# Performance work log

Hardware: AMD Instinct MI355X
Metric: run time of the kernel (lower is better)

The kernel has to match this reference:

```python
import jax, jax.numpy as jnp
import numpy as np

N = 40000          # nodes
E = 640000         # edges (avg degree 16)
F_IN = 128         # num_node_features
H = 64             # hidden_channels
C_OUT = 32         # num_classes


def _glorot(key, fan_in, fan_out):
    lim = np.sqrt(6.0 / (fan_in + fan_out)).astype(np.float32)
    return jax.random.uniform(key, (fan_in, fan_out), jnp.float32, -lim, lim)


def setup_inputs() -> dict:
    key = jax.random.key(0)
    ks = jax.random.split(key, 12)
    x = jax.random.normal(ks[0], (N, F_IN), jnp.float32)
    edge_index = jax.random.randint(ks[1], (2, E), 0, N, dtype=jnp.int32)
    batch = jnp.zeros((N,), jnp.int32)  # unused by forward, kept for signature fidelity
    return {
        "x": x,
        "edge_index": edge_index,
        "batch": batch,
        "W1": _glorot(ks[2], F_IN, H),      "b1": jnp.zeros((H,), jnp.float32),
        "W2": _glorot(ks[3], H, 2 * H),     "b2": jnp.zeros((2 * H,), jnp.float32),
        "W3": _glorot(ks[4], 2 * H, 2 * H), "b3": jnp.zeros((2 * H,), jnp.float32),
        "W4": _glorot(ks[5], 2 * H, H),     "b4": jnp.zeros((H,), jnp.float32),
        "Wl": _glorot(ks[6], H, C_OUT),     "bl": jnp.zeros((C_OUT,), jnp.float32),
    }


def _gcn_norm(edge_index, n_nodes):
    """Add self-loops and compute symmetric D^{-1/2} A D^{-1/2} edge weights."""
    loop = jnp.arange(n_nodes, dtype=edge_index.dtype)
    src = jnp.concatenate([edge_index[0], loop])
    dst = jnp.concatenate([edge_index[1], loop])
    deg = jax.ops.segment_sum(jnp.ones_like(dst, dtype=jnp.float32), dst,
                              num_segments=n_nodes)
    d_inv_sqrt = jnp.where(deg > 0, jax.lax.rsqrt(deg), 0.0)
    norm = d_inv_sqrt[src] * d_inv_sqrt[dst]  # [E + N]
    return src, dst, norm


def _gcn_conv(h, W, b, src, dst, norm, n_nodes):
    h = h @ W                                   # [N, d_out] linear transform first
    msg = h[src] * norm[:, None]                # gather + edge scaling
    agg = jax.ops.segment_sum(msg, dst, num_segments=n_nodes)  # scatter-add
    return agg + b


def reference(x, edge_index, batch, W1, b1, W2, b2, W3, b3, W4, b4, Wl, bl):
    n_nodes = x.shape[0]
    src, dst, norm = _gcn_norm(edge_index, n_nodes)
    # eval mode: F.dropout(training=False) is identity
    h = jax.nn.relu(_gcn_conv(x, W1, b1, src, dst, norm, n_nodes))
    h = jax.nn.relu(_gcn_conv(h, W2, b2, src, dst, norm, n_nodes))
    h = jax.nn.relu(_gcn_conv(h, W3, b3, src, dst, norm, n_nodes))
    h = jax.nn.relu(_gcn_conv(h, W4, b4, src, dst, norm, n_nodes))
    return h @ Wl + bl  # [N, C_OUT]
```

## Files before the change

kernel.cpp:

```cpp
#include <hip/hip_runtime.h>
#include <hip/hip_bf16.h>


using bf16x8 = __attribute__((ext_vector_type(8))) __bf16;
using f32x4  = __attribute__((ext_vector_type(4))) float;

__device__ __forceinline__ int block_detect_bf16(const unsigned short* __restrict__ x16) {
    __shared__ int cnt;
    if (threadIdx.x == 0) cnt = 0;
    __syncthreads();
    if (threadIdx.x < 128) {
        unsigned e = (x16[2 * threadIdx.x] >> 7) & 0xFF;
        if (e >= 100 && e <= 135) atomicAdd(&cnt, 1);
    }
    __syncthreads();
    return cnt >= 64;
}

struct PrepDesc { const void* src; void* dst; int n; int mode; int dol2; int strideK; };
struct PrepArgs { PrepDesc d[12]; int pre[13]; int ndesc; };

__global__ __launch_bounds__(256) void setup(PrepArgs a,
                                             const unsigned short* __restrict__ x16,
                                             int* __restrict__ flagG,
                                             const int* __restrict__ dstE,
                                             int* __restrict__ count, int E) {
    const int b = blockIdx.x;
    const int npre = a.pre[a.ndesc];
    if (b >= npre) {
        int e = (b - npre) * 256 + threadIdx.x;
        if (e < E) atomicAdd(&count[dstE[e]], 1);
        return;
    }
    const int fl = block_detect_bf16(x16);
    if (b == 0 && threadIdx.x == 0) *flagG = fl;
    int s = 0;
    for (; s < a.ndesc - 1; ++s) if (b < a.pre[s + 1]) break;
    const PrepDesc d = a.d[s];
    int i = (b - a.pre[s]) * 256 + threadIdx.x;
    if (i >= d.n) return;
    float v = fl ? __bfloat162float(((const __hip_bfloat16*)d.src)[i])
                 : ((const float*)d.src)[i];
    if (d.mode == 0) {
        ((float*)d.dst)[i] = v;
    } else {
        int k = i >> d.dol2;
        int col = i & ((1 << d.dol2) - 1);
        ((__hip_bfloat16*)d.dst)[col * d.strideK + k] = __float2bfloat16(v);
    }
}

__global__ __launch_bounds__(256) void scan_part(const int* __restrict__ count,
                                                 int* __restrict__ blockSums, int N) {
    __shared__ int red[256];
    const int t = threadIdx.x;
    const int i = (blockIdx.x << 8) + t;
    red[t] = (i < N) ? (count[i] + 7) & ~7 : 0;
    __syncthreads();
    for (int off = 128; off > 0; off >>= 1) {
        if (t < off) red[t] += red[t + off];
        __syncthreads();
    }
    if (t == 0) blockSums[blockIdx.x] = red[0];
}

__global__ __launch_bounds__(256) void scan_final(const int* __restrict__ count,
                                                  const int* __restrict__ blockSums,
                                                  int* __restrict__ rowptr,
                                                  int* __restrict__ bukCursor,
                                                  float* __restrict__ dinv,
                                                  int N) {
    __shared__ int lds[256];
    __shared__ int sOff;
    const int t = threadIdx.x;
    const int i = (blockIdx.x << 8) + t;
    const int c = (i < N) ? count[i] : 0;
    const int cp = (c + 7) & ~7;
    lds[t] = cp;
    __syncthreads();
    for (int off = 1; off < 256; off <<= 1) {
        int v = (t >= off) ? lds[t - off] : 0;
        __syncthreads();
        lds[t] += v;
        __syncthreads();
    }
    if (t == 0) {
        int o = 0;
        for (int b = 0; b < (int)blockIdx.x; ++b) o += blockSums[b];
        sOff = o;
    }
    __syncthreads();
    const int run = sOff + lds[t] - cp;
    if (i < N) {
        rowptr[i] = run;
        dinv[i] = rsqrtf((float)(c + 1));
        if ((i & 255) == 0) bukCursor[i >> 8] = run;
        if (i == N - 1) rowptr[N] = run + cp;
    }
}

__global__ __launch_bounds__(256) void bucket_scatter(const unsigned* __restrict__ staging,
                                                      const int* __restrict__ bukCursor,
                                                      const int* __restrict__ rowptr,
                                                      unsigned short* __restrict__ csr16,
                                                      int N) {
    __shared__ int cur[256];
    const int t = threadIdx.x;
    const int nb0 = blockIdx.x << 8;
    const int i = nb0 + t;
    cur[t] = (i < N) ? rowptr[i] : 0;
    __syncthreads();
    const int base = rowptr[nb0];
    const int m = bukCursor[blockIdx.x] - base;
    for (int k = t; k < m; k += 256) {
        unsigned e = staging[base + k];
        int loc = (e >> 16) & 255;
        int pos = atomicAdd(&cur[loc], 1);
        csr16[pos] = (unsigned short)(e & 0xffff);
    }
    __syncthreads();
    if (i < N) {
        const int end = rowptr[i + 1];
        for (int p = cur[t]; p < end; ++p) csr16[p] = (unsigned short)N;
    }
}

template<int W>
__device__ __forceinline__ void gather_acc8(const __hip_bfloat16* __restrict__ Hin,
                                            int cb, int node,
                                            const int* __restrict__ rowptr,
                                            const unsigned short* __restrict__ csr16,
                                            float acc[8]) {
    const __hip_bfloat16* base = Hin + cb;
    auto loadrow = [&](int s) -> uint4 {
        return *(const uint4*)(base + (size_t)s * W);
    };
    #pragma unroll
    for (int j = 0; j < 8; ++j) acc[j] = 0.f;
    auto accum = [&](uint4 u) {
        union { uint4 v; __hip_bfloat162 h2[4]; } c;
        c.v = u;
        #pragma unroll
        for (int j = 0; j < 4; ++j) {
            float2 p = __bfloat1622float2(c.h2[j]);
            acc[2 * j] += p.x;
            acc[2 * j + 1] += p.y;
        }
    };
    accum(loadrow(node));
    int e = rowptr[node];
    const int e1 = rowptr[node + 1];
    for (; e + 16 <= e1; e += 16) {
        union { uint4 v; unsigned short s[8]; } iv0, iv1;
        iv0.v = *(const uint4*)(csr16 + e);
        iv1.v = *(const uint4*)(csr16 + e + 8);
        uint4 r0 = loadrow(iv0.s[0]), r1 = loadrow(iv0.s[1]);
        uint4 r2 = loadrow(iv0.s[2]), r3 = loadrow(iv0.s[3]);
        uint4 r4 = loadrow(iv0.s[4]), r5 = loadrow(iv0.s[5]);
        uint4 r6 = loadrow(iv0.s[6]), r7 = loadrow(iv0.s[7]);
        uint4 r8 = loadrow(iv1.s[0]), r9 = loadrow(iv1.s[1]);
        uint4 ra = loadrow(iv1.s[2]), rb = loadrow(iv1.s[3]);
        uint4 rc = loadrow(iv1.s[4]), rd = loadrow(iv1.s[5]);
        uint4 re = loadrow(iv1.s[6]), rf = loadrow(iv1.s[7]);
        accum(r0); accum(r1); accum(r2); accum(r3);
        accum(r4); accum(r5); accum(r6); accum(r7);
        accum(r8); accum(r9); accum(ra); accum(rb);
        accum(rc); accum(rd); accum(re); accum(rf);
    }
    if (e < e1) {
        union { uint4 v; unsigned short s[8]; } iv;
        iv.v = *(const uint4*)(csr16 + e);
        uint4 r0 = loadrow(iv.s[0]), r1 = loadrow(iv.s[1]);
        uint4 r2 = loadrow(iv.s[2]), r3 = loadrow(iv.s[3]);
        uint4 r4 = loadrow(iv.s[4]), r5 = loadrow(iv.s[5]);
        uint4 r6 = loadrow(iv.s[6]), r7 = loadrow(iv.s[7]);
        accum(r0); accum(r1); accum(r2); accum(r3);
        accum(r4); accum(r5); accum(r6); accum(r7);
    }
}

__device__ __forceinline__ void zero_pad_row_b(__hip_bfloat16* zrow, int zn, bool lead) {
    if (zrow && lead) {
        for (int i = threadIdx.x * 8; i < zn; i += 2048)
            *(uint4*)(zrow + i) = make_uint4(0, 0, 0, 0);
    }
}

template<bool BIAS_RELU, bool POST_SCALE>
__global__ __launch_bounds__(256) void gather8(const __hip_bfloat16* __restrict__ Hin,
                                               const int* __restrict__ rowptr,
                                               const unsigned short* __restrict__ csr16,
                                               const float* __restrict__ dinv,
                                               const float* __restrict__ b,
                                               __hip_bfloat16* __restrict__ out, int n,
                                               __hip_bfloat16* zrow, int zn) {
    zero_pad_row_b(zrow, zn, blockIdx.x == 0);
    const int t = blockIdx.x * 256 + threadIdx.x;
    const int node = t >> 3;
    const int f = t & 7;
    if (node >= n) return;
    const int cb = f * 8;
    const float di = dinv[node];
    float acc[8];
    gather_acc8<64>(Hin, cb, node, rowptr, csr16, acc);
    union { uint4 v; __hip_bfloat16 h[8]; } p;
    #pragma unroll
    for (int j = 0; j < 8; ++j) {
        float v = di * acc[j];
        if (BIAS_RELU) v = fmaxf(v + b[cb + j], 0.f);
        if (POST_SCALE) v *= di;
        p.h[j] = __float2bfloat16(v);
    }
    *(uint4*)(out + (size_t)node * 64 + cb) = p.v;
}

template<int NTPW, bool BIAS_RELU, bool SCALE_ROW, bool RAW_A>
__device__ __forceinline__ void gemm_core(const void* __restrict__ Ain,
                                          const __hip_bfloat16* __restrict__ WT,
                                          const float* __restrict__ bias,
                                          const float* __restrict__ dinv,
                                          __hip_bfloat16* __restrict__ out,
                                          int d_in, int d_out_log2, int strideK,
                                          bool bfmode, int blk, int tid) {
    const int wave = tid >> 6, lane = tid & 63;
    const int m = lane & 15, quad = lane >> 4;
    const int rowBase = blk * 64;
    const int nkc = d_in >> 5;
    const int nt0 = wave * NTPW;

    f32x4 acc[4][NTPW];
    #pragma unroll
    for (int rt = 0; rt < 4; ++rt)
        #pragma unroll
        for (int j = 0; j < NTPW; ++j)
            acc[rt][j] = (f32x4){0.f, 0.f, 0.f, 0.f};

    auto mainloop = [&](bool asBF) {
        for (int kc = 0; kc < nkc; ++kc) {
            const int koff = (kc << 5) + quad * 8;
            bf16x8 a[4];
            #pragma unroll
            for (int rt = 0; rt < 4; ++rt) {
                const size_t off = (size_t)(rowBase + rt * 16 + m) * d_in + koff;
                if (!RAW_A || asBF) {
                    a[rt] = *(const bf16x8*)((const __hip_bfloat16*)Ain + off);
                } else {
                    const float* p = (const float*)Ain + off;
                    float4 f0 = *(const float4*)p;
                    float4 f1 = *(const float4*)(p + 4);
                    union { bf16x8 v; __hip_bfloat16 h[8]; } u;
                    u.h[0] = __float2bfloat16(f0.x); u.h[1] = __float2bfloat16(f0.y);
                    u.h[2] = __float2bfloat16(f0.z); u.h[3] = __float2bfloat16(f0.w);
                    u.h[4] = __float2bfloat16(f1.x); u.h[5] = __float2bfloat16(f1.y);
                    u.h[6] = __float2bfloat16(f1.z); u.h[7] = __float2bfloat16(f1.w);
                    a[rt] = u.v;
                }
            }
            #pragma unroll
            for (int j = 0; j < NTPW; ++j) {
                const int n = ((nt0 + j) << 4) + m;
                bf16x8 b = *(const bf16x8*)&WT[n * strideK + koff];
                #pragma unroll
                for (int rt = 0; rt < 4; ++rt)
                    acc[rt][j] = __builtin_amdgcn_mfma_f32_16x16x32_bf16(a[rt], b, acc[rt][j], 0, 0, 0);
            }
        }
    };
    if (bfmode) mainloop(true); else mainloop(false);

    const int d_out = 1 << d_out_log2;
    #pragma unroll
    for (int rt = 0; rt < 4; ++rt) {
        const int row = rowBase + rt * 16 + quad * 4;
        #pragma unroll
        for (int j = 0; j < NTPW; ++j) {
            const int col = ((nt0 + j) << 4) + m;
            float bv = BIAS_RELU ? bias[col] : 0.f;
            #pragma unroll
            for (int r = 0; r < 4; ++r) {
                float v = acc[rt][j][r];
                if (BIAS_RELU) v = fmaxf(v + bv, 0.f);
                if (SCALE_ROW) v *= dinv[row + r];
                out[(size_t)(row + r) * d_out + col] = __float2bfloat16(v);
            }
        }
    }
}

__global__ __launch_bounds__(256) void stage_gemm(const int* __restrict__ src,
                                                  const int* __restrict__ dst,
                                                  int E, int NBUK,
                                                  int* __restrict__ bukCursor,
                                                  unsigned* __restrict__ staging,
                                                  const void* __restrict__ Ain,
                                                  const __hip_bfloat16* __restrict__ WT,
                                                  const float* __restrict__ dinv,
                                                  __hip_bfloat16* __restrict__ out,
                                                  int strideK, const int* __restrict__ flag,
                                                  __hip_bfloat16* zrow, int zn, int SB) {
    if (blockIdx.x < SB) {
        __shared__ int hist[160], start[160], run[160];
        const int t = threadIdx.x;
        const int base = blockIdx.x * 4096;
        int sv[16], dv[16];
        #pragma unroll
        for (int j = 0; j < 16; ++j) {
            int e = base + j * 256 + t;
            if (e < E) { sv[j] = src[e]; dv[j] = dst[e]; } else dv[j] = -1;
        }
        if (t < NBUK) { hist[t] = 0; run[t] = 0; }
        __syncthreads();
        #pragma unroll
        for (int j = 0; j < 16; ++j)
            if (dv[j] >= 0) atomicAdd(&hist[dv[j] >> 8], 1);
        __syncthreads();
        if (t < NBUK && hist[t] > 0)
            start[t] = atomicAdd(&bukCursor[t], hist[t]);
        __syncthreads();
        #pragma unroll
        for (int j = 0; j < 16; ++j) {
            if (dv[j] >= 0) {
                int b = dv[j] >> 8;
                int slot = start[b] + atomicAdd(&run[b], 1);
                staging[slot] = ((unsigned)dv[j] << 16) | (unsigned)sv[j];
            }
        }
        return;
    }
    const int blk = blockIdx.x - SB;
    zero_pad_row_b(zrow, zn, blk == 0);
    const bool bfmode = (*flag != 0);
    gemm_core<1, false, true, true>(Ain, WT, nullptr, dinv, out, 128, 6, strideK,
                                    bfmode, blk, threadIdx.x);
}

template<int D_IN, int NTPW, bool BIAS_RELU, bool SCALE_ROW>
__global__ __launch_bounds__(256) void gather_gemm(const __hip_bfloat16* __restrict__ Hin,
                                                   const int* __restrict__ rowptr,
                                                   const unsigned short* __restrict__ csr16,
                                                   const float* __restrict__ dinv,
                                                   const __hip_bfloat16* __restrict__ WT,
                                                   const float* __restrict__ bias,
                                                   __hip_bfloat16* __restrict__ out,
                                                   int d_out_log2,
                                                   __hip_bfloat16* zrow, int zn) {
    zero_pad_row_b(zrow, zn, blockIdx.x == 0);
    constexpr int SK = D_IN + 8;
    __shared__ __align__(16) __hip_bfloat16 sG[64 * SK];
    const int tid = threadIdx.x;

    const int rowBase = blockIdx.x * 64;
    constexpr int TPR = D_IN / 8;
    constexpr int NPP = 256 / TPR;
    #pragma unroll
    for (int pass = 0; pass < 64 / NPP; ++pass) {
        const int local = pass * NPP + tid / TPR;
        const int node = rowBase + local;
        const int cb = (tid % TPR) * 8;
        float acc[8];
        gather_acc8<D_IN>(Hin, cb, node, rowptr, csr16, acc);
        const float di = dinv[node];
        union { bf16x8 v; __hip_bfloat16 h[8]; } p;
        #pragma unroll
        for (int j = 0; j < 8; ++j) p.h[j] = __float2bfloat16(di * acc[j]);
        *(bf16x8*)&sG[local * SK + cb] = p.v;
    }
    __syncthreads();

    const int wave = tid >> 6, lane = tid & 63;
    const int m = lane & 15, quad = lane >> 4;
    const int nkc = D_IN >> 5;
    const int nt0 = wave * NTPW;

    f32x4 acc2[4][NTPW];
    #pragma unroll
    for (int rt = 0; rt < 4; ++rt)
        #pragma unroll
        for (int j = 0; j < NTPW; ++j)
            acc2[rt][j] = (f32x4){0.f, 0.f, 0.f, 0.f};

    for (int kc = 0; kc < nkc; ++kc) {
        const int koff = (kc << 5) + quad * 8;
        bf16x8 a[4];
        #pragma unroll
        for (int rt = 0; rt < 4; ++rt)
            a[rt] = *(const bf16x8*)&sG[(rt * 16 + m) * SK + koff];
        #pragma unroll
        for (int j = 0; j < NTPW; ++j) {
            const int n = ((nt0 + j) << 4) + m;
            bf16x8 b = *(const bf16x8*)&WT[n * SK + koff];
            #pragma unroll
            for (int rt = 0; rt < 4; ++rt)
                acc2[rt][j] = __builtin_amdgcn_mfma_f32_16x16x32_bf16(a[rt], b, acc2[rt][j], 0, 0, 0);
        }
    }

    const int d_out = 1 << d_out_log2;
    #pragma unroll
    for (int rt = 0; rt < 4; ++rt) {
        const int row = rowBase + rt * 16 + quad * 4;
        #pragma unroll
        for (int j = 0; j < NTPW; ++j) {
            const int col = ((nt0 + j) << 4) + m;
            float bv = BIAS_RELU ? bias[col] : 0.f;
            #pragma unroll
            for (int r = 0; r < 4; ++r) {
                float v = acc2[rt][j][r];
                if (BIAS_RELU) v = fmaxf(v + bv, 0.f);
                if (SCALE_ROW) v *= dinv[row + r];
                out[(size_t)(row + r) * d_out + col] = __float2bfloat16(v);
            }
        }
    }
}

__global__ __launch_bounds__(256) void gather_gemm34(const __hip_bfloat16* __restrict__ Hin,
                                                     const int* __restrict__ rowptr,
                                                     const unsigned short* __restrict__ csr16,
                                                     const float* __restrict__ dinv,
                                                     const __hip_bfloat16* __restrict__ WT3,
                                                     const float* __restrict__ b3,
                                                     const __hip_bfloat16* __restrict__ WT4,
                                                     __hip_bfloat16* __restrict__ lin4,
                                                     __hip_bfloat16* zrow, int zn) {
    zero_pad_row_b(zrow, zn, blockIdx.x == 0);
    constexpr int SK = 136;
    __shared__ __align__(16) __hip_bfloat16 sG[64 * SK];
    const int tid = threadIdx.x;
    const int rowBase = blockIdx.x * 64;

    #pragma unroll
    for (int pass = 0; pass < 4; ++pass) {
        const int local = pass * 16 + tid / 16;
        const int node = rowBase + local;
        const int cb = (tid % 16) * 8;
        float acc[8];
        gather_acc8<128>(Hin, cb, node, rowptr, csr16, acc);
        const float di = dinv[node];
        union { bf16x8 v; __hip_bfloat16 h[8]; } p;
        #pragma unroll
        for (int j = 0; j < 8; ++j) p.h[j] = __float2bfloat16(di * acc[j]);
        *(bf16x8*)&sG[local * SK + cb] = p.v;
    }
    __syncthreads();

    const int wave = tid >> 6, lane = tid & 63;
    const int m = lane & 15, quad = lane >> 4;

    f32x4 acc2[4][2];
    #pragma unroll
    for (int rt = 0; rt < 4; ++rt)
        #pragma unroll
        for (int j = 0; j < 2; ++j)
            acc2[rt][j] = (f32x4){0.f, 0.f, 0.f, 0.f};
    for (int kc = 0; kc < 4; ++kc) {
        const int koff = (kc << 5) + quad * 8;
        bf16x8 a[4];
        #pragma unroll
        for (int rt = 0; rt < 4; ++rt)
            a[rt] = *(const bf16x8*)&sG[(rt * 16 + m) * SK + koff];
        #pragma unroll
        for (int j = 0; j < 2; ++j) {
            const int n = ((wave * 2 + j) << 4) + m;
            bf16x8 b = *(const bf16x8*)&WT3[n * SK + koff];
            #pragma unroll
            for (int rt = 0; rt < 4; ++rt)
                acc2[rt][j] = __builtin_amdgcn_mfma_f32_16x16x32_bf16(a[rt], b, acc2[rt][j], 0, 0, 0);
        }
    }
    __syncthreads();

    #pragma unroll
    for (int j = 0; j < 2; ++j) {
        const int col = ((wave * 2 + j) << 4) + m;
        const float bv = b3[col];
        #pragma unroll
        for (int rt = 0; rt < 4; ++rt) {
            const int row = rt * 16 + quad * 4;
            #pragma unroll
            for (int r = 0; r < 4; ++r)
                sG[(row + r) * SK + col] = __float2bfloat16(fmaxf(acc2[rt][j][r] + bv, 0.f));
        }
    }
    __syncthreads();

    f32x4 acc3[4];
    #pragma unroll
    for (int rt = 0; rt < 4; ++rt) acc3[rt] = (f32x4){0.f, 0.f, 0.f, 0.f};
    for (int kc = 0; kc < 4; ++kc) {
        const int koff = (kc << 5) + quad * 8;
        bf16x8 a[4];
        #pragma unroll
        for (int rt = 0; rt < 4; ++rt)
            a[rt] = *(const bf16x8*)&sG[(rt * 16 + m) * SK + koff];
        const int n = (wave << 4) + m;
        bf16x8 b = *(const bf16x8*)&WT4[n * SK + koff];
        #pragma unroll
        for (int rt = 0; rt < 4; ++rt)
            acc3[rt] = __builtin_amdgcn_mfma_f32_16x16x32_bf16(a[rt], b, acc3[rt], 0, 0, 0);
    }

    const int col = (wave << 4) + m;
    #pragma unroll
    for (int rt = 0; rt < 4; ++rt) {
        const int row = rowBase + rt * 16 + quad * 4;
        #pragma unroll
        for (int r = 0; r < 4; ++r)
            lin4[(size_t)(row + r) * 64 + col] = __float2bfloat16(acc3[rt][r] * dinv[row + r]);
    }
}

__global__ __launch_bounds__(256) void gather_final(const __hip_bfloat16* __restrict__ Hin,
                                                    const int* __restrict__ rowptr,
                                                    const unsigned short* __restrict__ csr16,
                                                    const float* __restrict__ dinv,
                                                    const float* __restrict__ b4,
                                                    const float* __restrict__ Wlf,
                                                    const float* __restrict__ blf,
                                                    void* __restrict__ out,
                                                    const int* __restrict__ flag) {
    __shared__ float sWl[64 * 32];
    __shared__ float sH[32 * 65];
    const int tid = threadIdx.x;
    for (int i = tid; i < 2048; i += 256) sWl[i] = Wlf[i];
    const int nl = tid >> 3, j = tid & 7, cb = j * 8;
    const int node = blockIdx.x * 32 + nl;
    float acc[8];
    gather_acc8<64>(Hin, cb, node, rowptr, csr16, acc);
    const float di = dinv[node];
    #pragma unroll
    for (int k = 0; k < 8; ++k)
        sH[nl * 65 + cb + k] = fmaxf(di * acc[k] + b4[cb + k], 0.f);
    __syncthreads();
    float4 r = *(const float4*)(blf + 4 * j);
    for (int k = 0; k < 64; ++k) {
        const float hv = sH[nl * 65 + k];
        const float4 w = *(const float4*)&sWl[k * 32 + 4 * j];
        r.x += hv * w.x; r.y += hv * w.y; r.z += hv * w.z; r.w += hv * w.w;
    }
    const size_t idx = (size_t)node * 32 + 4 * j;
    if (*flag) {
        union { __hip_bfloat16 h[4]; uint2 u; } p;
        p.h[0] = __float2bfloat16(r.x); p.h[1] = __float2bfloat16(r.y);
        p.h[2] = __float2bfloat16(r.z); p.h[3] = __float2bfloat16(r.w);
        *(uint2*)((__hip_bfloat16*)out + idx) = p.u;
    } else {
        *(float4*)((float*)out + idx) = r;
    }
}

extern "C" void kernel_launch(void* const* d_in, const int* in_sizes, int n_in,
                              void* d_out, int out_size, void* d_ws, size_t ws_size,
                              hipStream_t stream) {
    const int* edge = (const int*)d_in[1];
    const int F_IN = 128;
    const int N = in_sizes[0] / F_IN;
    const int E = in_sizes[1] / 2;
    const int* src = edge;
    const int* dst = edge + E;
    const int NBUK = (N + 255) >> 8;

    auto align256 = [](size_t v) { return (v + 255) & ~(size_t)255; };
    char* ws = (char*)d_ws;
    int*   flag    = (int*)ws;    ws += 256;
    float* dinv    = (float*)ws;  ws += align256((size_t)N * 4);
    int*   count   = (int*)ws;    ws += align256((size_t)N * 4);
    int*   rowptr  = (int*)ws;    ws += align256((size_t)(N + 1) * 4);
    int*   bukCursor = (int*)ws;  ws += align256((size_t)NBUK * 4);
    int*   blockSums = (int*)ws;  ws += align256((size_t)NBUK * 4);
    unsigned short* csr16 = (unsigned short*)ws; ws += align256(((size_t)E + 8 * N + 64) * 2);
    unsigned* staging = (unsigned*)ws; ws += align256(((size_t)E + 8 * N + 64) * 4);
    __hip_bfloat16* Hbuf = (__hip_bfloat16*)ws; ws += align256(((size_t)N + 1) * 128 * 2);
    __hip_bfloat16* Tbuf = (__hip_bfloat16*)ws; ws += align256(((size_t)N + 1) * 128 * 2);

    const int widx[4] = {3, 5, 7, 9};
    const int bidx[4] = {4, 6, 8, 10};
    float* Bc[4];
    for (int i = 0; i < 4; ++i) { Bc[i] = (float*)ws; ws += align256((size_t)in_sizes[bidx[i]] * 4); }
    float* Wlf = (float*)ws; ws += align256((size_t)in_sizes[11] * 4);
    float* blf = (float*)ws; ws += align256((size_t)in_sizes[12] * 4);

    const int LD_IN[4]  = {128, 64, 128, 128};
    const int LD_OL2[4] = {6, 7, 7, 6};
    int strideK[4];
    __hip_bfloat16* WT[4];
    for (int l = 0; l < 4; ++l) {
        strideK[l] = LD_IN[l] + 8;
        WT[l] = (__hip_bfloat16*)ws;
        ws += align256((size_t)(1 << LD_OL2[l]) * strideK[l] * 2);
    }

    hipMemsetAsync(count, 0, (size_t)N * 4, stream);

    PrepArgs pa{};
    int nd = 0, pre = 0;
    auto addDesc = [&](const void* s, void* d, int n, int mode, int dol2, int sk) {
        pa.d[nd] = {s, d, n, mode, dol2, sk};
        pa.pre[nd] = pre;
        pre += (n + 255) / 256;
        nd++;
    };
    for (int l = 0; l < 4; ++l)
        addDesc(d_in[widx[l]], WT[l], LD_IN[l] << LD_OL2[l], 1, LD_OL2[l], strideK[l]);
    for (int l = 0; l < 4; ++l)
        addDesc(d_in[bidx[l]], Bc[l], in_sizes[bidx[l]], 0, 0, 0);
    addDesc(d_in[11], Wlf, in_sizes[11], 0, 0, 0);
    addDesc(d_in[12], blf, in_sizes[12], 0, 0, 0);
    pa.pre[nd] = pre;
    pa.ndesc = nd;
    const int EB = (E + 255) / 256;
    setup<<<pre + EB, 256, 0, stream>>>(pa, (const unsigned short*)d_in[0], flag, dst, count, E);

    scan_part<<<NBUK, 256, 0, stream>>>(count, blockSums, N);
    scan_final<<<NBUK, 256, 0, stream>>>(count, blockSums, rowptr, bukCursor, dinv, N);

    const int nblk = N / 64;
    const int g64  = (N * 8 + 255) / 256;
    const int SB   = (E + 4095) / 4096;

    stage_gemm<<<SB + nblk, 256, 0, stream>>>(
        src, dst, E, NBUK, bukCursor, staging,
        d_in[0], WT[0], dinv, Tbuf, strideK[0], flag, Tbuf + (size_t)N * 64, 64, SB);

    bucket_scatter<<<NBUK, 256, 0, stream>>>(staging, bukCursor, rowptr, csr16, N);

    gather8<true, true><<<g64, 256, 0, stream>>>(
        Tbuf, rowptr, csr16, dinv, Bc[0], Hbuf, N, Hbuf + (size_t)N * 64, 64);

    gather_gemm<64, 2, true, true><<<nblk, 256, 0, stream>>>(
        Hbuf, rowptr, csr16, dinv, WT[1], Bc[1], Tbuf, 7, Tbuf + (size_t)N * 128, 128);

    gather_gemm34<<<nblk, 256, 0, stream>>>(
        Tbuf, rowptr, csr16, dinv, WT[2], Bc[2], WT[3], Hbuf,
        Hbuf + (size_t)N * 64, 64);

    gather_final<<<g64, 256, 0, stream>>>(
        Hbuf, rowptr, csr16, dinv, Bc[3], Wlf, blf, d_out, flag);
}
```

Baseline: 220.8 us.

## Bucket edges by fixed-capacity buckets, fuse CSR build, store per-edge norm weights

The CSR build is reorganised. Edges are binned into fixed-capacity per-bucket staging regions first. The degree histogram, dinv and block sums are then computed from those buckets in the same launch as the first GEMM, and the scan and scatter are merged into one kernel. This removes the global count atomics and several launches. The CSR entries grow from 16 to 32 bits and carry a bf16 copy of the source node's dinv, so the gathers apply per-edge weights instead of relying on pre-scaled rows. That doubles index traffic, rounds the weights to bf16, and assumes each bucket fits within BUKCAP.

Result: faster. 200.9 us (-9.0%).

```diff
diff --git a/kernel.cpp b/kernel.cpp
--- a/kernel.cpp
+++ b/kernel.cpp
@@ -4,6 +4,8 @@
 
 using bf16x8 = __attribute__((ext_vector_type(8))) __bf16;
 using f32x4  = __attribute__((ext_vector_type(4))) float;
+
+#define BUKCAP 8192
 
 __device__ __forceinline__ int block_detect_bf16(const unsigned short* __restrict__ x16) {
     __shared__ int cnt;
@@ -20,16 +22,43 @@
 struct PrepDesc { const void* src; void* dst; int n; int mode; int dol2; int strideK; };
 struct PrepArgs { PrepDesc d[12]; int pre[13]; int ndesc; };
 
-__global__ __launch_bounds__(256) void setup(PrepArgs a,
-                                             const unsigned short* __restrict__ x16,
-                                             int* __restrict__ flagG,
-                                             const int* __restrict__ dstE,
-                                             int* __restrict__ count, int E) {
+__global__ __launch_bounds__(256) void prep_stage(PrepArgs a,
+                                                  const unsigned short* __restrict__ x16,
+                                                  int* __restrict__ flagG,
+                                                  const int* __restrict__ src,
+                                                  const int* __restrict__ dst,
+                                                  int E, int NBUK,
+                                                  int* __restrict__ bukFill,
+                                                  unsigned* __restrict__ staging) {
     const int b = blockIdx.x;
     const int npre = a.pre[a.ndesc];
     if (b >= npre) {
-        int e = (b - npre) * 256 + threadIdx.x;
-        if (e < E) atomicAdd(&count[dstE[e]], 1);
+        __shared__ int hist[160], start[160], run[160];
+        const int t = threadIdx.x;
+        const int base = (b - npre) * 4096;
+        int sv[16], dv[16];
+        #pragma unroll
+        for (int j = 0; j < 16; ++j) {
+            int e = base + j * 256 + t;
+            if (e < E) { sv[j] = src[e]; dv[j] = dst[e]; } else dv[j] = -1;
+        }
+        if (t < NBUK) { hist[t] = 0; run[t] = 0; }
+        __syncthreads();
+        #pragma unroll
+        for (int j = 0; j < 16; ++j)
+            if (dv[j] >= 0) atomicAdd(&hist[dv[j] >> 8], 1);
+        __syncthreads();
+        if (t < NBUK && hist[t] > 0)
+            start[t] = atomicAdd(&bukFill[t], hist[t]);
+        __syncthreads();
+        #pragma unroll
+        for (int j = 0; j < 16; ++j) {
+            if (dv[j] >= 0) {
+                int bk = dv[j] >> 8;
+                int slot = start[bk] + atomicAdd(&run[bk], 1);
+                staging[(size_t)bk * BUKCAP + slot] = ((unsigned)dv[j] << 16) | (unsigned)sv[j];
+            }
+        }
         return;
     }
     const int fl = block_detect_bf16(x16);
@@ -50,175 +79,10 @@
     }
 }
 
-__global__ __launch_bounds__(256) void scan_part(const int* __restrict__ count,
-                                                 int* __restrict__ blockSums, int N) {
-    __shared__ int red[256];
-    const int t = threadIdx.x;
-    const int i = (blockIdx.x << 8) + t;
-    red[t] = (i < N) ? (count[i] + 7) & ~7 : 0;
-    __syncthreads();
-    for (int off = 128; off > 0; off >>= 1) {
-        if (t < off) red[t] += red[t + off];
-        __syncthreads();
-    }
-    if (t == 0) blockSums[blockIdx.x] = red[0];
-}
-
-__global__ __launch_bounds__(256) void scan_final(const int* __restrict__ count,
-                                                  const int* __restrict__ blockSums,
-                                                  int* __restrict__ rowptr,
-                                                  int* __restrict__ bukCursor,
-                                                  float* __restrict__ dinv,
-                                                  int N) {
-    __shared__ int lds[256];
-    __shared__ int sOff;
-    const int t = threadIdx.x;
-    const int i = (blockIdx.x << 8) + t;
-    const int c = (i < N) ? count[i] : 0;
-    const int cp = (c + 7) & ~7;
-    lds[t] = cp;
-    __syncthreads();
-    for (int off = 1; off < 256; off <<= 1) {
-        int v = (t >= off) ? lds[t - off] : 0;
-        __syncthreads();
-        lds[t] += v;
-        __syncthreads();
-    }
-    if (t == 0) {
-        int o = 0;
-        for (int b = 0; b < (int)blockIdx.x; ++b) o += blockSums[b];
-        sOff = o;
-    }
-    __syncthreads();
-    const int run = sOff + lds[t] - cp;
-    if (i < N) {
-        rowptr[i] = run;
-        dinv[i] = rsqrtf((float)(c + 1));
-        if ((i & 255) == 0) bukCursor[i >> 8] = run;
-        if (i == N - 1) rowptr[N] = run + cp;
-    }
-}
-
-__global__ __launch_bounds__(256) void bucket_scatter(const unsigned* __restrict__ staging,
-                                                      const int* __restrict__ bukCursor,
-                                                      const int* __restrict__ rowptr,
-                                                      unsigned short* __restrict__ csr16,
-                                                      int N) {
-    __shared__ int cur[256];
-    const int t = threadIdx.x;
-    const int nb0 = blockIdx.x << 8;
-    const int i = nb0 + t;
-    cur[t] = (i < N) ? rowptr[i] : 0;
-    __syncthreads();
-    const int base = rowptr[nb0];
-    const int m = bukCursor[blockIdx.x] - base;
-    for (int k = t; k < m; k += 256) {
-        unsigned e = staging[base + k];
-        int loc = (e >> 16) & 255;
-        int pos = atomicAdd(&cur[loc], 1);
-        csr16[pos] = (unsigned short)(e & 0xffff);
-    }
-    __syncthreads();
-    if (i < N) {
-        const int end = rowptr[i + 1];
-        for (int p = cur[t]; p < end; ++p) csr16[p] = (unsigned short)N;
-    }
-}
-
-template<int W>
-__device__ __forceinline__ void gather_acc8(const __hip_bfloat16* __restrict__ Hin,
-                                            int cb, int node,
-                                            const int* __restrict__ rowptr,
-                                            const unsigned short* __restrict__ csr16,
-                                            float acc[8]) {
-    const __hip_bfloat16* base = Hin + cb;
-    auto loadrow = [&](int s) -> uint4 {
-        return *(const uint4*)(base + (size_t)s * W);
-    };
-    #pragma unroll
-    for (int j = 0; j < 8; ++j) acc[j] = 0.f;
-    auto accum = [&](uint4 u) {
-        union { uint4 v; __hip_bfloat162 h2[4]; } c;
-        c.v = u;
-        #pragma unroll
-        for (int j = 0; j < 4; ++j) {
-            float2 p = __bfloat1622float2(c.h2[j]);
-            acc[2 * j] += p.x;
-            acc[2 * j + 1] += p.y;
-        }
-    };
-    accum(loadrow(node));
-    int e = rowptr[node];
-    const int e1 = rowptr[node + 1];
-    for (; e + 16 <= e1; e += 16) {
-        union { uint4 v; unsigned short s[8]; } iv0, iv1;
-        iv0.v = *(const uint4*)(csr16 + e);
-        iv1.v = *(const uint4*)(csr16 + e + 8);
-        uint4 r0 = loadrow(iv0.s[0]), r1 = loadrow(iv0.s[1]);
-        uint4 r2 = loadrow(iv0.s[2]), r3 = loadrow(iv0.s[3]);
-        uint4 r4 = loadrow(iv0.s[4]), r5 = loadrow(iv0.s[5]);
-        uint4 r6 = loadrow(iv0.s[6]), r7 = loadrow(iv0.s[7]);
-        uint4 r8 = loadrow(iv1.s[0]), r9 = loadrow(iv1.s[1]);
-        uint4 ra = loadrow(iv1.s[2]), rb = loadrow(iv1.s[3]);
-        uint4 rc = loadrow(iv1.s[4]), rd = loadrow(iv1.s[5]);
-        uint4 re = loadrow(iv1.s[6]), rf = loadrow(iv1.s[7]);
-        accum(r0); accum(r1); accum(r2); accum(r3);
-        accum(r4); accum(r5); accum(r6); accum(r7);
-        accum(r8); accum(r9); accum(ra); accum(rb);
-        accum(rc); accum(rd); accum(re); accum(rf);
-    }
-    if (e < e1) {
-        union { uint4 v; unsigned short s[8]; } iv;
-        iv.v = *(const uint4*)(csr16 + e);
-        uint4 r0 = loadrow(iv.s[0]), r1 = loadrow(iv.s[1]);
-        uint4 r2 = loadrow(iv.s[2]), r3 = loadrow(iv.s[3]);
-        uint4 r4 = loadrow(iv.s[4]), r5 = loadrow(iv.s[5]);
-        uint4 r6 = loadrow(iv.s[6]), r7 = loadrow(iv.s[7]);
-        accum(r0); accum(r1); accum(r2); accum(r3);
-        accum(r4); accum(r5); accum(r6); accum(r7);
-    }
-}
-
-__device__ __forceinline__ void zero_pad_row_b(__hip_bfloat16* zrow, int zn, bool lead) {
-    if (zrow && lead) {
-        for (int i = threadIdx.x * 8; i < zn; i += 2048)
-            *(uint4*)(zrow + i) = make_uint4(0, 0, 0, 0);
-    }
-}
-
-template<bool BIAS_RELU, bool POST_SCALE>
-__global__ __launch_bounds__(256) void gather8(const __hip_bfloat16* __restrict__ Hin,
-                                               const int* __restrict__ rowptr,
-                                               const unsigned short* __restrict__ csr16,
-                                               const float* __restrict__ dinv,
-                                               const float* __restrict__ b,
-                                               __hip_bfloat16* __restrict__ out, int n,
-                                               __hip_bfloat16* zrow, int zn) {
-    zero_pad_row_b(zrow, zn, blockIdx.x == 0);
-    const int t = blockIdx.x * 256 + threadIdx.x;
-    const int node = t >> 3;
-    const int f = t & 7;
-    if (node >= n) return;
-    const int cb = f * 8;
-    const float di = dinv[node];
-    float acc[8];
-    gather_acc8<64>(Hin, cb, node, rowptr, csr16, acc);
-    union { uint4 v; __hip_bfloat16 h[8]; } p;
-    #pragma unroll
-    for (int j = 0; j < 8; ++j) {
-        float v = di * acc[j];
-        if (BIAS_RELU) v = fmaxf(v + b[cb + j], 0.f);
-        if (POST_SCALE) v *= di;
-        p.h[j] = __float2bfloat16(v);
-    }
-    *(uint4*)(out + (size_t)node * 64 + cb) = p.v;
-}
-
-template<int NTPW, bool BIAS_RELU, bool SCALE_ROW, bool RAW_A>
+template<int NTPW, bool BIAS_RELU, bool RAW_A>
 __device__ __forceinline__ void gemm_core(const void* __restrict__ Ain,
                                           const __hip_bfloat16* __restrict__ WT,
                                           const float* __restrict__ bias,
-                                          const float* __restrict__ dinv,
                                           __hip_bfloat16* __restrict__ out,
                                           int d_in, int d_out_log2, int strideK,
                                           bool bfmode, int blk, int tid) {
@@ -280,75 +144,190 @@
             for (int r = 0; r < 4; ++r) {
                 float v = acc[rt][j][r];
                 if (BIAS_RELU) v = fmaxf(v + bv, 0.f);
-                if (SCALE_ROW) v *= dinv[row + r];
                 out[(size_t)(row + r) * d_out + col] = __float2bfloat16(v);
             }
         }
     }
 }
 
-__global__ __launch_bounds__(256) void stage_gemm(const int* __restrict__ src,
-                                                  const int* __restrict__ dst,
-                                                  int E, int NBUK,
-                                                  int* __restrict__ bukCursor,
-                                                  unsigned* __restrict__ staging,
-                                                  const void* __restrict__ Ain,
-                                                  const __hip_bfloat16* __restrict__ WT,
-                                                  const float* __restrict__ dinv,
-                                                  __hip_bfloat16* __restrict__ out,
-                                                  int strideK, const int* __restrict__ flag,
-                                                  __hip_bfloat16* zrow, int zn, int SB) {
-    if (blockIdx.x < SB) {
-        __shared__ int hist[160], start[160], run[160];
+__global__ __launch_bounds__(256) void hist_gemm(const unsigned* __restrict__ staging,
+                                                 const int* __restrict__ bukFill,
+                                                 int* __restrict__ count,
+                                                 float* __restrict__ dinv,
+                                                 int* __restrict__ blockSums,
+                                                 int N, int NBUK,
+                                                 const void* __restrict__ x,
+                                                 const __hip_bfloat16* __restrict__ WT0,
+                                                 __hip_bfloat16* __restrict__ lin1,
+                                                 int strideK0,
+                                                 const int* __restrict__ flag) {
+    if ((int)blockIdx.x < NBUK) {
+        __shared__ int hist[256];
+        __shared__ int red[256];
         const int t = threadIdx.x;
-        const int base = blockIdx.x * 4096;
-        int sv[16], dv[16];
-        #pragma unroll
-        for (int j = 0; j < 16; ++j) {
-            int e = base + j * 256 + t;
-            if (e < E) { sv[j] = src[e]; dv[j] = dst[e]; } else dv[j] = -1;
-        }
-        if (t < NBUK) { hist[t] = 0; run[t] = 0; }
-        __syncthreads();
-        #pragma unroll
-        for (int j = 0; j < 16; ++j)
-            if (dv[j] >= 0) atomicAdd(&hist[dv[j] >> 8], 1);
-        __syncthreads();
-        if (t < NBUK && hist[t] > 0)
-            start[t] = atomicAdd(&bukCursor[t], hist[t]);
-        __syncthreads();
-        #pragma unroll
-        for (int j = 0; j < 16; ++j) {
-            if (dv[j] >= 0) {
-                int b = dv[j] >> 8;
-                int slot = start[b] + atomicAdd(&run[b], 1);
-                staging[slot] = ((unsigned)dv[j] << 16) | (unsigned)sv[j];
-            }
-        }
+        hist[t] = 0;
+        __syncthreads();
+        const int fill = bukFill[blockIdx.x];
+        const unsigned* st = staging + (size_t)blockIdx.x * BUKCAP;
+        for (int k = t; k < fill; k += 256)
+            atomicAdd(&hist[(st[k] >> 16) & 255], 1);
+        __syncthreads();
+        const int i = (blockIdx.x << 8) + t;
+        const int c = hist[t];
+        if (i < N) {
+            count[i] = c;
+            dinv[i] = rsqrtf((float)(c + 1));
+        }
+        red[t] = (i < N) ? (c + 7) & ~7 : 0;
+        __syncthreads();
+        for (int off = 128; off > 0; off >>= 1) {
+            if (t < off) red[t] += red[t + off];
+            __syncthreads();
+        }
+        if (t == 0) blockSums[blockIdx.x] = red[0];
         return;
     }
-    const int blk = blockIdx.x - SB;
-    zero_pad_row_b(zrow, zn, blk == 0);
-    const bool bfmode = (*flag != 0);
-    gemm_core<1, false, true, true>(Ain, WT, nullptr, dinv, out, 128, 6, strideK,
-                                    bfmode, blk, threadIdx.x);
-}
-
-template<int D_IN, int NTPW, bool BIAS_RELU, bool SCALE_ROW>
+    gemm_core<1, false, true>(x, WT0, nullptr, lin1, 128, 6, strideK0,
+                              (*flag != 0), blockIdx.x - NBUK, threadIdx.x);
+}
+
+__global__ __launch_bounds__(256) void scan_scatter(const int* __restrict__ count,
+                                                    const int* __restrict__ blockSums,
+                                                    const int* __restrict__ bukFill,
+                                                    const unsigned* __restrict__ staging,
+                                                    const float* __restrict__ dinv,
+                                                    int* __restrict__ rowptr,
+                                                    unsigned* __restrict__ csr32,
+                                                    int N) {
+    __shared__ int lds[256];
+    __shared__ int cur[256];
+    __shared__ int sOff;
+    const int t = threadIdx.x;
+    const int i = (blockIdx.x << 8) + t;
+    const int c = (i < N) ? count[i] : 0;
+    const int cp = (c + 7) & ~7;
+    lds[t] = cp;
+    __syncthreads();
+    for (int off = 1; off < 256; off <<= 1) {
+        int v = (t >= off) ? lds[t - off] : 0;
+        __syncthreads();
+        lds[t] += v;
+        __syncthreads();
+    }
+    if (t == 0) {
+        int o = 0;
+        for (int b = 0; b < (int)blockIdx.x; ++b) o += blockSums[b];
+        sOff = o;
+    }
+    __syncthreads();
+    const int run = sOff + lds[t] - cp;
+    cur[t] = run;
+    if (i < N) {
+        rowptr[i] = run;
+        if (i == N - 1) rowptr[N] = run + cp;
+    }
+    __syncthreads();
+    const int fill = bukFill[blockIdx.x];
+    const unsigned* st = staging + (size_t)blockIdx.x * BUKCAP;
+    for (int k = t; k < fill; k += 256) {
+        unsigned u = st[k];
+        int s = (int)(u & 0xffffu);
+        int loc = (u >> 16) & 255;
+        int pos = atomicAdd(&cur[loc], 1);
+        union { __hip_bfloat16 h; unsigned short w16; } cv;
+        cv.h = __float2bfloat16(dinv[s]);
+        csr32[pos] = ((unsigned)cv.w16 << 16) | (unsigned)s;
+    }
+    __syncthreads();
+    const int pe = run + cp;
+    for (int p = cur[t]; p < pe; ++p) csr32[p] = 0u;
+}
+
+template<int W>
+__device__ __forceinline__ void gather_acc8w(const __hip_bfloat16* __restrict__ Hin,
+                                             int cb, int node, float di,
+                                             const int* __restrict__ rowptr,
+                                             const unsigned* __restrict__ csr32,
+                                             float acc[8]) {
+    const __hip_bfloat16* base = Hin + cb;
+    auto loadrow = [&](unsigned u) -> uint4 {
+        return *(const uint4*)(base + (size_t)(u & 0xffffu) * W);
+    };
+    auto wof = [](unsigned u) -> float {
+        return __int_as_float((int)(u & 0xffff0000u));
+    };
+    auto accumw = [&](uint4 v, float w) {
+        union { uint4 q; __hip_bfloat162 h2[4]; } c;
+        c.q = v;
+        #pragma unroll
+        for (int j = 0; j < 4; ++j) {
+            float2 p = __bfloat1622float2(c.h2[j]);
+            acc[2 * j]     += w * p.x;
+            acc[2 * j + 1] += w * p.y;
+        }
+    };
+    #pragma unroll
+    for (int j = 0; j < 8; ++j) acc[j] = 0.f;
+    accumw(*(const uint4*)(base + (size_t)node * W), di);
+    int e = rowptr[node];
+    const int e1 = rowptr[node + 1];
+    for (; e + 16 <= e1; e += 16) {
+        uint4 i0 = *(const uint4*)(csr32 + e);
+        uint4 i1 = *(const uint4*)(csr32 + e + 4);
+        uint4 i2 = *(const uint4*)(csr32 + e + 8);
+        uint4 i3 = *(const uint4*)(csr32 + e + 12);
+        uint4 r0 = loadrow(i0.x), r1 = loadrow(i0.y), r2 = loadrow(i0.z), r3 = loadrow(i0.w);
+        uint4 r4 = loadrow(i1.x), r5 = loadrow(i1.y), r6 = loadrow(i1.z), r7 = loadrow(i1.w);
+        uint4 r8 = loadrow(i2.x), r9 = loadrow(i2.y), ra = loadrow(i2.z), rb = loadrow(i2.w);
+        uint4 rc = loadrow(i3.x), rd = loadrow(i3.y), re = loadrow(i3.z), rf = loadrow(i3.w);
+        accumw(r0, wof(i0.x)); accumw(r1, wof(i0.y)); accumw(r2, wof(i0.z)); accumw(r3, wof(i0.w));
+        accumw(r4, wof(i1.x)); accumw(r5, wof(i1.y)); accumw(r6, wof(i1.z)); accumw(r7, wof(i1.w));
+        accumw(r8, wof(i2.x)); accumw(r9, wof(i2.y)); accumw(ra, wof(i2.z)); accumw(rb, wof(i2.w));
+        accumw(rc, wof(i3.x)); accumw(rd, wof(i3.y)); accumw(re, wof(i3.z)); accumw(rf, wof(i3.w));
+    }
+    if (e < e1) {
+        uint4 i0 = *(const uint4*)(csr32 + e);
+        uint4 i1 = *(const uint4*)(csr32 + e + 4);
+        uint4 r0 = loadrow(i0.x), r1 = loadrow(i0.y), r2 = loadrow(i0.z), r3 = loadrow(i0.w);
+        uint4 r4 = loadrow(i1.x), r5 = loadrow(i1.y), r6 = loadrow(i1.z), r7 = loadrow(i1.w);
+        accumw(r0, wof(i0.x)); accumw(r1, wof(i0.y)); accumw(r2, wof(i0.z)); accumw(r3, wof(i0.w));
+        accumw(r4, wof(i1.x)); accumw(r5, wof(i1.y)); accumw(r6, wof(i1.z)); accumw(r7, wof(i1.w));
+    }
+}
+
+__global__ __launch_bounds__(256) void gather8(const __hip_bfloat16* __restrict__ Hin,
+                                               const int* __restrict__ rowptr,
+                                               const unsigned* __restrict__ csr32,
+                                               const float* __restrict__ dinv,
+                                               const float* __restrict__ b,
+                                               __hip_bfloat16* __restrict__ out, int n) {
+    const int t = blockIdx.x * 256 + threadIdx.x;
+    const int node = t >> 3;
+    const int f = t & 7;
+    if (node >= n) return;
+    const int cb = f * 8;
+    const float di = dinv[node];
+    float acc[8];
+    gather_acc8w<64>(Hin, cb, node, di, rowptr, csr32, acc);
+    union { uint4 v; __hip_bfloat16 h[8]; } p;
+    #pragma unroll
+    for (int j = 0; j < 8; ++j)
+        p.h[j] = __float2bfloat16(fmaxf(di * acc[j] + b[cb + j], 0.f));
+    *(uint4*)(out + (size_t)node * 64 + cb) = p.v;
+}
+
+template<int D_IN, int NTPW>
 __global__ __launch_bounds__(256) void gather_gemm(const __hip_bfloat16* __restrict__ Hin,
                                                    const int* __restrict__ rowptr,
-                                                   const unsigned short* __restrict__ csr16,
+                                                   const unsigned* __restrict__ csr32,
                                                    const float* __restrict__ dinv,
                                                    const __hip_bfloat16* __restrict__ WT,
                                                    const float* __restrict__ bias,
                                                    __hip_bfloat16* __restrict__ out,
-                                                   int d_out_log2,
-                                                   __hip_bfloat16* zrow, int zn) {
-    zero_pad_row_b(zrow, zn, blockIdx.x == 0);
+                                                   int d_out_log2) {
     constexpr int SK = D_IN + 8;
     __shared__ __align__(16) __hip_bfloat16 sG[64 * SK];
     const int tid = threadIdx.x;
-
     const int rowBase = blockIdx.x * 64;
     constexpr int TPR = D_IN / 8;
     constexpr int NPP = 256 / TPR;
@@ -357,9 +336,9 @@
         const int local = pass * NPP + tid / TPR;
         const int node = rowBase + local;
         const int cb = (tid % TPR) * 8;
+        const float di = dinv[node];
         float acc[8];
-        gather_acc8<D_IN>(Hin, cb, node, rowptr, csr16, acc);
-        const float di = dinv[node];
+        gather_acc8w<D_IN>(Hin, cb, node, di, rowptr, csr32, acc);
         union { bf16x8 v; __hip_bfloat16 h[8]; } p;
         #pragma unroll
         for (int j = 0; j < 8; ++j) p.h[j] = __float2bfloat16(di * acc[j]);
@@ -402,28 +381,23 @@
         #pragma unroll
         for (int j = 0; j < NTPW; ++j) {
             const int col = ((nt0 + j) << 4) + m;
-            float bv = BIAS_RELU ? bias[col] : 0.f;
+            const float bv = bias[col];
             #pragma unroll
-            for (int r = 0; r < 4; ++r) {
-                float v = acc2[rt][j][r];
-                if (BIAS_RELU) v = fmaxf(v + bv, 0.f);
-                if (SCALE_ROW) v *= dinv[row + r];
-                out[(size_t)(row + r) * d_out + col] = __float2bfloat16(v);
-            }
+            for (int r = 0; r < 4; ++r)
+                out[(size_t)(row + r) * d_out + col] =
+                    __float2bfloat16(fmaxf(acc2[rt][j][r] + bv, 0.f));
         }
     }
 }
 
 __global__ __launch_bounds__(256) void gather_gemm34(const __hip_bfloat16* __restrict__ Hin,
                                                      const int* __restrict__ rowptr,
-                                                     const unsigned short* __restrict__ csr16,
+                                                     const unsigned* __restrict__ csr32,
                                                      const float* __restrict__ dinv,
                                                      const __hip_bfloat16* __restrict__ WT3,
                                                      const float* __restrict__ b3,
                                                      const __hip_bfloat16* __restrict__ WT4,
-                                                     __hip_bfloat16* __restrict__ lin4,
-                                                     __hip_bfloat16* zrow, int zn) {
-    zero_pad_row_b(zrow, zn, blockIdx.x == 0);
+                                                     __hip_bfloat16* __restrict__ lin4) {
     constexpr int SK = 136;
     __shared__ __align__(16) __hip_bfloat16 sG[64 * SK];
     const int tid = threadIdx.x;
@@ -434,9 +408,9 @@
         const int local = pass * 16 + tid / 16;
         const int node = rowBase + local;
         const int cb = (tid % 16) * 8;
+        const float di = dinv[node];
         float acc[8];
-        gather_acc8<128>(Hin, cb, node, rowptr, csr16, acc);
-        const float di = dinv[node];
+        gather_acc8w<128>(Hin, cb, node, di, rowptr, csr32, acc);
         union { bf16x8 v; __hip_bfloat16 h[8]; } p;
         #pragma unroll
         for (int j = 0; j < 8; ++j) p.h[j] = __float2bfloat16(di * acc[j]);
@@ -499,20 +473,19 @@
         for (int rt = 0; rt < 4; ++rt)
             acc3[rt] = __builtin_amdgcn_mfma_f32_16x16x32_bf16(a[rt], b, acc3[rt], 0, 0, 0);
     }
-
     const int col = (wave << 4) + m;
     #pragma unroll
     for (int rt = 0; rt < 4; ++rt) {
         const int row = rowBase + rt * 16 + quad * 4;
         #pragma unroll
         for (int r = 0; r < 4; ++r)
-            lin4[(size_t)(row + r) * 64 + col] = __float2bfloat16(acc3[rt][r] * dinv[row + r]);
+            lin4[(size_t)(row + r) * 64 + col] = __float2bfloat16(acc3[rt][r]);
     }
 }
 
 __global__ __launch_bounds__(256) void gather_final(const __hip_bfloat16* __restrict__ Hin,
                                                     const int* __restrict__ rowptr,
-                                                    const unsigned short* __restrict__ csr16,
+                                                    const unsigned* __restrict__ csr32,
                                                     const float* __restrict__ dinv,
                                                     const float* __restrict__ b4,
                                                     const float* __restrict__ Wlf,
@@ -525,9 +498,9 @@
     for (int i = tid; i < 2048; i += 256) sWl[i] = Wlf[i];
     const int nl = tid >> 3, j = tid & 7, cb = j * 8;
     const int node = blockIdx.x * 32 + nl;
+    const float di = dinv[node];
     float acc[8];
-    gather_acc8<64>(Hin, cb, node, rowptr, csr16, acc);
-    const float di = dinv[node];
+    gather_acc8w<64>(Hin, cb, node, di, rowptr, csr32, acc);
     #pragma unroll
     for (int k = 0; k < 8; ++k)
         sH[nl * 65 + cb + k] = fmaxf(di * acc[k] + b4[cb + k], 0.f);
@@ -566,12 +539,12 @@
     float* dinv    = (float*)ws;  ws += align256((size_t)N * 4);
     int*   count   = (int*)ws;    ws += align256((size_t)N * 4);
     int*   rowptr  = (int*)ws;    ws += align256((size_t)(N + 1) * 4);
-    int*   bukCursor = (int*)ws;  ws += align256((size_t)NBUK * 4);
+    int*   bukFill = (int*)ws;    ws += align256((size_t)NBUK * 4);
     int*   blockSums = (int*)ws;  ws += align256((size_t)NBUK * 4);
-    unsigned short* csr16 = (unsigned short*)ws; ws += align256(((size_t)E + 8 * N + 64) * 2);
-    unsigned* staging = (unsigned*)ws; ws += align256(((size_t)E + 8 * N + 64) * 4);
-    __hip_bfloat16* Hbuf = (__hip_bfloat16*)ws; ws += align256(((size_t)N + 1) * 128 * 2);
-    __hip_bfloat16* Tbuf = (__hip_bfloat16*)ws; ws += align256(((size_t)N + 1) * 128 * 2);
+    unsigned* csr32   = (unsigned*)ws; ws += align256(((size_t)E + 8 * N + 64) * 4);
+    unsigned* staging = (unsigned*)ws; ws += align256((size_t)NBUK * BUKCAP * 4);
+    __hip_bfloat16* Hbuf = (__hip_bfloat16*)ws; ws += align256((size_t)N * 128 * 2);
+    __hip_bfloat16* Tbuf = (__hip_bfloat16*)ws; ws += align256((size_t)N * 128 * 2);
 
     const int widx[4] = {3, 5, 7, 9};
     const int bidx[4] = {4, 6, 8, 10};
@@ -590,7 +563,7 @@
         ws += align256((size_t)(1 << LD_OL2[l]) * strideK[l] * 2);
     }
 
-    hipMemsetAsync(count, 0, (size_t)N * 4, stream);
+    hipMemsetAsync(bukFill, 0, (size_t)NBUK * 4, stream);
 
     PrepArgs pa{};
     int nd = 0, pre = 0;
@@ -608,32 +581,24 @@
     addDesc(d_in[12], blf, in_sizes[12], 0, 0, 0);
     pa.pre[nd] = pre;
     pa.ndesc = nd;
-    const int EB = (E + 255) / 256;
-    setup<<<pre + EB, 256, 0, stream>>>(pa, (const unsigned short*)d_in[0], flag, dst, count, E);
-
-    scan_part<<<NBUK, 256, 0, stream>>>(count, blockSums, N);
-    scan_final<<<NBUK, 256, 0, stream>>>(count, blockSums, rowptr, bukCursor, dinv, N);
+    const int SB = (E + 4095) / 4096;
+    prep_stage<<<pre + SB, 256, 0, stream>>>(pa, (const unsigned short*)d_in[0], flag,
+                                             src, dst, E, NBUK, bukFill, staging);
 
     const int nblk = N / 64;
     const int g64  = (N * 8 + 255) / 256;
-    const int SB   = (E + 4095) / 4096;
-
-    stage_gemm<<<SB + nblk, 256, 0, stream>>>(
-        src, dst, E, NBUK, bukCursor, staging,
-        d_in[0], WT[0], dinv, Tbuf, strideK[0], flag, Tbuf + (size_t)N * 64, 64, SB);
-
-    bucket_scatter<<<NBUK, 256, 0, stream>>>(staging, bukCursor, rowptr, csr16, N);
-
-    gather8<true, true><<<g64, 256, 0, stream>>>(
-        Tbuf, rowptr, csr16, dinv, Bc[0], Hbuf, N, Hbuf + (size_t)N * 64, 64);
-
-    gather_gemm<64, 2, true, true><<<nblk, 256, 0, stream>>>(
-        Hbuf, rowptr, csr16, dinv, WT[1], Bc[1], Tbuf, 7, Tbuf + (size_t)N * 128, 128);
-
-    gather_gemm34<<<nblk, 256, 0, stream>>>(
-        Tbuf, rowptr, csr16, dinv, WT[2], Bc[2], WT[3], Hbuf,
-        Hbuf + (size_t)N * 64, 64);
-
-    gather_final<<<g64, 256, 0, stream>>>(
-        Hbuf, rowptr, csr16, dinv, Bc[3], Wlf, blf, d_out, flag);
-}
+
+    hist_gemm<<<NBUK + nblk, 256, 0, stream>>>(staging, bukFill, count, dinv, blockSums,
+                                               N, NBUK, d_in[0], WT[0], Tbuf, strideK[0], flag);
+
+    scan_scatter<<<NBUK, 256, 0, stream>>>(count, blockSums, bukFill, staging, dinv,
+                                           rowptr, csr32, N);
+
+    gather8<<<g64, 256, 0, stream>>>(Tbuf, rowptr, csr32, dinv, Bc[0], Hbuf, N);
+
+    gather_gemm<64, 2><<<nblk, 256, 0, stream>>>(Hbuf, rowptr, csr32, dinv, WT[1], Bc[1], Tbuf, 7);
+
+    gather_gemm34<<<nblk, 256, 0, stream>>>(Tbuf, rowptr, csr32, dinv, WT[2], Bc[2], WT[3], Hbuf);
+
+    gather_final<<<g64, 256, 0, stream>>>(Hbuf, rowptr, csr32, dinv, Bc[3], Wlf, blf, d_out, flag);
+}
```
